# Optimization experiments

Measured on AMD Instinct MI355X. Metric: run time of the kernel, lower is better.

The kernel has to match this reference:

```python
import jax, jax.numpy as jnp
import numpy as np

SAMP_RATE = 48000.0
HARMONIC_NUM = 8
DIM = HARMONIC_NUM + 1
SINE_AMP = 0.1
NOISE_STD = 0.003
VOICED_THRESHOLD = 0.0

B, T, UPP = 4, 1500, 512


def _linear_upsample_align_corners(x, upp):
    # x: [B, T, D] -> [B, T*upp, D], matches F.interpolate(mode='linear', align_corners=True)
    b, t, d = x.shape
    t_out = t * upp
    pos = jnp.arange(t_out, dtype=jnp.float32) * (float(t - 1) / float(t_out - 1))
    i0 = jnp.floor(pos).astype(jnp.int32)
    i1 = jnp.minimum(i0 + 1, t - 1)
    w = (pos - i0.astype(jnp.float32))[None, :, None]
    return x[:, i0, :] * (1.0 - w) + x[:, i1, :] * w


def setup_inputs() -> dict:
    key = jax.random.key(0)
    k1, k2, k3, k4 = jax.random.split(key, 4)
    u1 = jax.random.uniform(k1, (B, T), dtype=jnp.float32)
    u2 = jax.random.uniform(k2, (B, T), dtype=jnp.float32)
    f0 = jnp.where(u2 < 0.15, 0.0, 80.0 + 320.0 * u1)
    # random initial phase per harmonic; fundamental (col 0) gets zero, per the source
    rand_ini = jax.random.uniform(k3, (B, DIM), dtype=jnp.float32)
    rand_ini = rand_ini.at[:, 0].set(0.0)
    # standard normal noise, replaces torch.randn_like(sine_waves)
    noise_z = jax.random.normal(k4, (B, T * UPP, DIM), dtype=jnp.float32)
    return {"f0": f0, "rand_ini": rand_ini, "noise_z": noise_z, "upp": UPP}


def reference(f0, rand_ini, noise_z, upp):
    # harmonics: fundamental * (1, 2, ..., DIM)
    mult = jnp.arange(1, DIM + 1, dtype=f0.dtype)            # [DIM]
    f0_buf = f0[:, :, None] * mult                           # [B, T, DIM]
    rad_values = (f0_buf / SAMP_RATE) % 1.0                  # per-frame phase increment (cycles)
    rad_values = rad_values.at[:, 0, :].add(rand_ini)        # random init phase at t=0

    tmp_over_one = jnp.cumsum(rad_values, axis=1) * upp      # [B, T, DIM]
    tmp_over_one = _linear_upsample_align_corners(tmp_over_one, upp) % 1.0  # [B, T*upp, DIM]
    rad_up = jnp.repeat(rad_values, upp, axis=1)             # nearest upsample, [B, T*upp, DIM]

    # detect phase wrap-around; subtract 1 cycle where the fractional phase dropped
    wrap = (tmp_over_one[:, 1:, :] - tmp_over_one[:, :-1, :]) < 0.0
    cumsum_shift = jnp.concatenate(
        [jnp.zeros_like(rad_up[:, :1, :]), jnp.where(wrap, -1.0, 0.0)], axis=1
    )
    phase = jnp.cumsum(rad_up + cumsum_shift, axis=1)
    sine_waves = jnp.sin(phase * (2.0 * np.pi)) * SINE_AMP

    uv = (f0 > VOICED_THRESHOLD).astype(f0.dtype)[:, :, None]  # [B, T, 1]
    uv = jnp.repeat(uv, upp, axis=1)                            # [B, T*upp, 1]

    noise_amp = uv * NOISE_STD + (1.0 - uv) * (SINE_AMP / 3.0)
    noise = noise_amp * noise_z
    sine_waves = sine_waves * uv + noise
    return sine_waves, uv, noise
```

## Files before the change

kernel.cpp:

```cpp
#include <hip/hip_runtime.h>

#define BB 4
#define TT 1500
#define UPP 512
#define DIMH 9
#define TUP (TT * UPP)
static_assert(TUP == 768000, "");
constexpr unsigned E_MAIN = (unsigned)BB * TUP * DIMH;
constexpr unsigned E_UV   = (unsigned)BB * TUP;
constexpr int MAIN_BLOCKS = (int)(E_MAIN / 8 / 256);
constexpr int UV_BLOCKS   = (int)(E_UV / 8 / 256);

__device__ __forceinline__ float sin2pi(float revs) {
#if __has_builtin(__builtin_amdgcn_sinf)
    return __builtin_amdgcn_sinf(revs);
#else
    return sinf(6.2831853071795864f * revs);
#endif
}

__global__ __launch_bounds__(256) void scan_kernel(
        const float* __restrict__ f0,
        const float* __restrict__ rand_ini,
        float* __restrict__ fr512, float* __restrict__ rad32) {
    const int bd = blockIdx.x;
    const int b = bd / DIMH, d = bd % DIMH;
    const int tid = threadIdx.x;
    const double mult = (double)(d + 1);
    const int base = tid * 6;

    double r[6];
    double tot = 0.0;
    #pragma unroll
    for (int e = 0; e < 6; ++e) {
        int t = base + e;
        double rv = 0.0;
        if (t < TT) {
            double x = (double)f0[b * TT + t] * mult / 48000.0;
            rv = x - floor(x);
            if (t == 0) rv += (double)rand_ini[b * DIMH + d];
        }
        r[e] = rv;
        tot += rv;
    }

    __shared__ double sd[256];
    sd[tid] = tot;
    __syncthreads();
    #pragma unroll
    for (int off = 1; off < 256; off <<= 1) {
        double v = (tid >= off) ? sd[tid - off] : 0.0;
        __syncthreads();
        sd[tid] += v;
        __syncthreads();
    }
    double run = sd[tid] - tot;

    #pragma unroll
    for (int e = 0; e < 6; ++e) {
        int t = base + e;
        if (t < TT) {
            double c = 512.0 * run;
            fr512[bd * TT + t] = (float)(c - floor(c));
            rad32[bd * TT + t] = (float)r[e];
        }
        run += r[e];
    }
}

__global__ __launch_bounds__(256) void main_kernel(
        const float* __restrict__ f0,
        const float* __restrict__ nz,
        const float* __restrict__ fr512, const float* __restrict__ rad32,
        float* __restrict__ out) {
    const int blk = blockIdx.x;
    const int tid = threadIdx.x;

    if (blk < MAIN_BLOCKS) {
        const unsigned k0 = ((unsigned)blk * 256u + (unsigned)tid) * 8u;

        const float4* zp = reinterpret_cast<const float4*>(nz + k0);
        float4 za = zp[0], zb = zp[1];
        float z[8] = {za.x, za.y, za.z, za.w, zb.x, zb.y, zb.z, zb.w};

        const unsigned s0 = k0 / 9u;
        const unsigned d0 = k0 - s0 * 9u;
        const unsigned sBi = min(s0 + 1u, (unsigned)(BB * TUP) - 1u);

        unsigned bA = s0 / (unsigned)TUP;
        unsigned iA = s0 - bA * (unsigned)TUP;
        unsigned tA = iA >> 9, jA = iA & 511u;
        float f0A = f0[bA * TT + tA];
        float uvA = (f0A > 0.0f) ? 1.0f : 0.0f;
        float namA = (f0A > 0.0f) ? 0.003f : (0.1f / 3.0f);
        unsigned baseA = (bA * 9u) * (unsigned)TT + tA;
        float jp1A = (float)(jA + 1u);

        unsigned bB = sBi / (unsigned)TUP;
        unsigned iB = sBi - bB * (unsigned)TUP;
        unsigned tB = iB >> 9, jB = iB & 511u;
        float f0B = f0[bB * TT + tB];
        float uvB = (f0B > 0.0f) ? 1.0f : 0.0f;
        float namB = (f0B > 0.0f) ? 0.003f : (0.1f / 3.0f);
        unsigned baseB = (bB * 9u) * (unsigned)TT + tB;
        float jp1B = (float)(jB + 1u);

        float o0[8], o2[8];
        unsigned d = d0;
        bool sec = false;
        #pragma unroll
        for (int e = 0; e < 8; ++e) {
            unsigned idx = (sec ? baseB : baseA) + d * (unsigned)TT;
            float jp1 = sec ? jp1B : jp1A;
            float ph = fr512[idx] + jp1 * rad32[idx];
            float fr = ph - floorf(ph);
            float sn = sin2pi(fr) * 0.1f;
            float uvv = sec ? uvB : uvA;
            float nam = sec ? namB : namA;
            float nse = nam * z[e];
            o0[e] = sn * uvv + nse;
            o2[e] = nse;
            if (++d == 9u) { d = 0u; sec = true; }
        }

        float4* so = reinterpret_cast<float4*>(out + k0);
        so[0] = make_float4(o0[0], o0[1], o0[2], o0[3]);
        so[1] = make_float4(o0[4], o0[5], o0[6], o0[7]);
        float4* no = reinterpret_cast<float4*>(out + (size_t)E_MAIN + E_UV + k0);
        no[0] = make_float4(o2[0], o2[1], o2[2], o2[3]);
        no[1] = make_float4(o2[4], o2[5], o2[6], o2[7]);
    } else {
        const unsigned g = ((unsigned)(blk - MAIN_BLOCKS) * 256u + (unsigned)tid) * 8u;
        float o1[8];
        #pragma unroll
        for (int e = 0; e < 8; ++e) {
            unsigned s = g + (unsigned)e;
            unsigned b = s / (unsigned)TUP;
            unsigned i = s - b * (unsigned)TUP;
            unsigned t = i >> 9;
            o1[e] = (f0[b * TT + t] > 0.0f) ? 1.0f : 0.0f;
        }
        float4* uo = reinterpret_cast<float4*>(out + (size_t)E_MAIN + g);
        uo[0] = make_float4(o1[0], o1[1], o1[2], o1[3]);
        uo[1] = make_float4(o1[4], o1[5], o1[6], o1[7]);
    }
}

extern "C" void kernel_launch(void* const* d_in, const int* in_sizes, int n_in,
                              void* d_out, int out_size, void* d_ws, size_t ws_size,
                              hipStream_t stream) {
    const float* f0       = (const float*)d_in[0];
    const float* rand_ini = (const float*)d_in[1];
    const float* noise_z  = (const float*)d_in[2];

    float* fr512 = (float*)d_ws;
    float* rad32 = fr512 + (size_t)BB * DIMH * TT;

    float* out = (float*)d_out;

    scan_kernel<<<BB * DIMH, 256, 0, stream>>>(f0, rand_ini, fr512, rad32);
    main_kernel<<<MAIN_BLOCKS + UV_BLOCKS, 256, 0, stream>>>(f0, noise_z, fr512, rad32, out);
}
```

Measured before the change: 358.8 us.

## Interleave phase tables, use wave-shuffle scan, and nontemporal streaming loads/stores

The scan kernel now runs as a single 64-lane wavefront per (batch, harmonic). Each lane handles 24 frames and uses shuffle-based prefix sums in place of a shared-memory scan with many barriers. The two per-frame tables are packed into one interleaved float2 array, so the main kernel fetches both values with one 8-byte load. Noise loads and all output stores now use nontemporal hints to limit cache pollution on the large streaming traffic. The risk is that the main kernel is bandwidth bound, so the scan and table changes may matter little, and nontemporal hints can help or hurt depending on how the hardware handles them.

```diff
diff --git a/kernel.cpp b/kernel.cpp
--- a/kernel.cpp
+++ b/kernel.cpp
@@ -11,6 +11,9 @@
 constexpr int MAIN_BLOCKS = (int)(E_MAIN / 8 / 256);
 constexpr int UV_BLOCKS   = (int)(E_UV / 8 / 256);
 
+typedef float  vf4 __attribute__((ext_vector_type(4)));
+typedef float  vf2 __attribute__((ext_vector_type(2)));
+
 __device__ __forceinline__ float sin2pi(float revs) {
 #if __has_builtin(__builtin_amdgcn_sinf)
     return __builtin_amdgcn_sinf(revs);
@@ -19,24 +22,25 @@
 #endif
 }
 
-__global__ __launch_bounds__(256) void scan_kernel(
+__global__ __launch_bounds__(64) void scan_kernel(
         const float* __restrict__ f0,
         const float* __restrict__ rand_ini,
-        float* __restrict__ fr512, float* __restrict__ rad32) {
+        vf2* __restrict__ tab) {
     const int bd = blockIdx.x;
     const int b = bd / DIMH, d = bd % DIMH;
-    const int tid = threadIdx.x;
+    const int lane = threadIdx.x;
     const double mult = (double)(d + 1);
-    const int base = tid * 6;
+    constexpr int PER = 24;
+    const int base = lane * PER;
 
-    double r[6];
+    double r[PER];
     double tot = 0.0;
     #pragma unroll
-    for (int e = 0; e < 6; ++e) {
+    for (int e = 0; e < PER; ++e) {
         int t = base + e;
         double rv = 0.0;
         if (t < TT) {
-            double x = (double)f0[b * TT + t] * mult / 48000.0;
+            double x = (double)f0[b * TT + t] * mult * (1.0 / 48000.0);
             rv = x - floor(x);
             if (t == 0) rv += (double)rand_ini[b * DIMH + d];
         }
@@ -44,25 +48,22 @@
         tot += rv;
     }
 
-    __shared__ double sd[256];
-    sd[tid] = tot;
-    __syncthreads();
+    double sum = tot;
     #pragma unroll
-    for (int off = 1; off < 256; off <<= 1) {
-        double v = (tid >= off) ? sd[tid - off] : 0.0;
-        __syncthreads();
-        sd[tid] += v;
-        __syncthreads();
+    for (int off = 1; off < 64; off <<= 1) {
+        double v = __shfl_up(sum, off, 64);
+        if (lane >= off) sum += v;
     }
-    double run = sd[tid] - tot;
+    double run = sum - tot;
 
     #pragma unroll
-    for (int e = 0; e < 6; ++e) {
+    for (int e = 0; e < PER; ++e) {
         int t = base + e;
         if (t < TT) {
             double c = 512.0 * run;
-            fr512[bd * TT + t] = (float)(c - floor(c));
-            rad32[bd * TT + t] = (float)r[e];
+            c -= floor(c);
+            vf2 v; v.x = (float)c; v.y = (float)r[e];
+            tab[bd * TT + t] = v;
         }
         run += r[e];
     }
@@ -71,7 +72,7 @@
 __global__ __launch_bounds__(256) void main_kernel(
         const float* __restrict__ f0,
         const float* __restrict__ nz,
-        const float* __restrict__ fr512, const float* __restrict__ rad32,
+        const vf2* __restrict__ tab,
         float* __restrict__ out) {
     const int blk = blockIdx.x;
     const int tid = threadIdx.x;
@@ -79,8 +80,9 @@
     if (blk < MAIN_BLOCKS) {
         const unsigned k0 = ((unsigned)blk * 256u + (unsigned)tid) * 8u;
 
-        const float4* zp = reinterpret_cast<const float4*>(nz + k0);
-        float4 za = zp[0], zb = zp[1];
+        const vf4* zp = reinterpret_cast<const vf4*>(nz + k0);
+        vf4 za = __builtin_nontemporal_load(zp);
+        vf4 zb = __builtin_nontemporal_load(zp + 1);
         float z[8] = {za.x, za.y, za.z, za.w, zb.x, zb.y, zb.z, zb.w};
 
         const unsigned s0 = k0 / 9u;
@@ -111,8 +113,9 @@
         #pragma unroll
         for (int e = 0; e < 8; ++e) {
             unsigned idx = (sec ? baseB : baseA) + d * (unsigned)TT;
+            vf2 fr_rad = tab[idx];
             float jp1 = sec ? jp1B : jp1A;
-            float ph = fr512[idx] + jp1 * rad32[idx];
+            float ph = fr_rad.x + jp1 * fr_rad.y;
             float fr = ph - floorf(ph);
             float sn = sin2pi(fr) * 0.1f;
             float uvv = sec ? uvB : uvA;
@@ -123,12 +126,16 @@
             if (++d == 9u) { d = 0u; sec = true; }
         }
 
-        float4* so = reinterpret_cast<float4*>(out + k0);
-        so[0] = make_float4(o0[0], o0[1], o0[2], o0[3]);
-        so[1] = make_float4(o0[4], o0[5], o0[6], o0[7]);
-        float4* no = reinterpret_cast<float4*>(out + (size_t)E_MAIN + E_UV + k0);
-        no[0] = make_float4(o2[0], o2[1], o2[2], o2[3]);
-        no[1] = make_float4(o2[4], o2[5], o2[6], o2[7]);
+        vf4* so = reinterpret_cast<vf4*>(out + k0);
+        vf4 s0v = {o0[0], o0[1], o0[2], o0[3]};
+        vf4 s1v = {o0[4], o0[5], o0[6], o0[7]};
+        __builtin_nontemporal_store(s0v, so);
+        __builtin_nontemporal_store(s1v, so + 1);
+        vf4* no = reinterpret_cast<vf4*>(out + (size_t)E_MAIN + E_UV + k0);
+        vf4 n0v = {o2[0], o2[1], o2[2], o2[3]};
+        vf4 n1v = {o2[4], o2[5], o2[6], o2[7]};
+        __builtin_nontemporal_store(n0v, no);
+        __builtin_nontemporal_store(n1v, no + 1);
     } else {
         const unsigned g = ((unsigned)(blk - MAIN_BLOCKS) * 256u + (unsigned)tid) * 8u;
         float o1[8];
@@ -140,9 +147,11 @@
             unsigned t = i >> 9;
             o1[e] = (f0[b * TT + t] > 0.0f) ? 1.0f : 0.0f;
         }
-        float4* uo = reinterpret_cast<float4*>(out + (size_t)E_MAIN + g);
-        uo[0] = make_float4(o1[0], o1[1], o1[2], o1[3]);
-        uo[1] = make_float4(o1[4], o1[5], o1[6], o1[7]);
+        vf4* uo = reinterpret_cast<vf4*>(out + (size_t)E_MAIN + g);
+        vf4 u0v = {o1[0], o1[1], o1[2], o1[3]};
+        vf4 u1v = {o1[4], o1[5], o1[6], o1[7]};
+        __builtin_nontemporal_store(u0v, uo);
+        __builtin_nontemporal_store(u1v, uo + 1);
     }
 }
 
@@ -153,11 +162,9 @@
     const float* rand_ini = (const float*)d_in[1];
     const float* noise_z  = (const float*)d_in[2];
 
-    float* fr512 = (float*)d_ws;
-    float* rad32 = fr512 + (size_t)BB * DIMH * TT;
-
+    vf2* tab = (vf2*)d_ws;
     float* out = (float*)d_out;
 
-    scan_kernel<<<BB * DIMH, 256, 0, stream>>>(f0, rand_ini, fr512, rad32);
-    main_kernel<<<MAIN_BLOCKS + UV_BLOCKS, 256, 0, stream>>>(f0, noise_z, fr512, rad32, out);
+    scan_kernel<<<BB * DIMH, 64, 0, stream>>>(f0, rand_ini, tab);
+    main_kernel<<<MAIN_BLOCKS + UV_BLOCKS, 256, 0, stream>>>(f0, noise_z, tab, out);
 }
```

Result: faster. 331.6 us (-7.6%).
